# Optimization experiments

Hardware: AMD Instinct MI355X
Metric: run time of the kernel (lower is better)

The kernel has to match this reference:

```python
import jax, jax.numpy as jnp
import numpy as np

N_NODES = 10000   # chain length (supply-chain echelons)
BATCH   = 32      # graphs per batch
F_IN    = 5       # node features: inventory, replenishment, last_repl, units_sold, lost_sales
HID     = 128     # hidden_dim
LN_EPS  = 1e-5


def setup_inputs() -> dict:
    key = jax.random.key(0)
    ks = jax.random.split(key, 8)
    state  = jax.random.normal(ks[0], (BATCH, N_NODES * 4), dtype=jnp.float32)
    action = jax.random.normal(ks[1], (BATCH, N_NODES), dtype=jnp.float32)
    # GCNConv params (W: [F_IN, HID], bias added after aggregation, PyG convention)
    conv_w = jax.random.normal(ks[2], (F_IN, HID), dtype=jnp.float32) / np.sqrt(F_IN)
    conv_b = jax.random.normal(ks[3], (HID,), dtype=jnp.float32) * 0.01
    ln_g = jnp.ones((HID,), jnp.float32)
    ln_b = jnp.zeros((HID,), jnp.float32)
    w2 = jax.random.normal(ks[4], (HID, HID), dtype=jnp.float32) / np.sqrt(HID)
    b2 = jax.random.normal(ks[5], (HID,), dtype=jnp.float32) * 0.01
    w3 = jax.random.normal(ks[6], (HID, 1), dtype=jnp.float32) / np.sqrt(HID)
    b3 = jax.random.normal(ks[7], (1,), dtype=jnp.float32) * 0.01
    # bidirectional chain edges + self loops (GCNConv add_self_loops=True)
    i = np.arange(N_NODES)
    src = np.concatenate([i[:-1], i[1:], i]).astype(np.int32)
    dst = np.concatenate([i[1:], i[:-1], i]).astype(np.int32)
    return {
        "state": state, "action": action,
        "conv_w": conv_w, "conv_b": conv_b,
        "ln_g": ln_g, "ln_b": ln_b,
        "w2": w2, "b2": b2, "w3": w3, "b3": b3,
        "src": jnp.asarray(src), "dst": jnp.asarray(dst),
        "bs": BATCH,
    }


def reference(state, action, conv_w, conv_b, ln_g, ln_b, w2, b2, w3, b3, src, dst, bs):
    # sa = cat([state, action], -1), each batch row reshaped to [N_NODES, F_IN] node features
    sa = jnp.concatenate([state, action], axis=-1).reshape(bs, N_NODES, F_IN)

    # GCNConv: symmetric normalization with self-loops.
    deg = jnp.zeros((N_NODES,), sa.dtype).at[dst].add(1.0)      # in-degree incl. self-loop
    norm = jax.lax.rsqrt(deg[src] * deg[dst])                   # [E]

    h = jnp.einsum('bnf,fh->bnh', sa, conv_w)                   # transform first (F_IN small)
    msgs = h[:, src, :] * norm[None, :, None]                   # gather along edges [B,E,H]
    agg = jnp.zeros_like(h).at[:, dst, :].add(msgs)             # scatter-add aggregate [B,N,H]
    x = jax.nn.relu(agg + conv_b)

    # LayerNorm over feature dim
    mu = jnp.mean(x, axis=-1, keepdims=True)
    var = jnp.mean((x - mu) ** 2, axis=-1, keepdims=True)
    xn = (x - mu) * jax.lax.rsqrt(var + LN_EPS) * ln_g + ln_b

    # global_add_pool with batch vector of all zeros: sum over every node of the batched graph
    pooled = jnp.sum(xn, axis=(0, 1))[None, :]                  # [1, HID]

    y = jax.nn.relu(pooled @ w2 + b2)
    return y @ w3 + b3                                          # [1, 1]
```

## Files before the change

### kernel.cpp

```cpp
#include <hip/hip_runtime.h>
#include <math.h>

#define N_NODES 10000
#define BATCH   32
#define F_IN    5
#define HID     128
#define LN_EPS  1e-5f
#define CHUNK   500
#define NB_PER_BATCH 20
#define NBLK (BATCH * NB_PER_BATCH)
#define CONCAT_N (N_NODES * F_IN)
#define STATE_N  (N_NODES * 4)
#define STAGE_F4 635

__global__ __launch_bounds__(256) void gcn_ln_pool_kernel(
    const float* __restrict__ state, const float* __restrict__ action,
    const float* __restrict__ conv_w, const float* __restrict__ conv_b,
    float* __restrict__ partial)
{
    __shared__ float s_sa[2560];
    __shared__ float s_red[4][HID];

    const int b     = blockIdx.x / NB_PER_BATCH;
    const int chunk = blockIdx.x % NB_PER_BATCH;
    const int n0    = chunk * CHUNK;
    const int t     = threadIdx.x;

    const int e0 = (n0 - 4) * F_IN;
    const float4* stv = (const float4*)(state  + b * STATE_N);
    const float4* acv = (const float4*)(action + b * N_NODES);
    for (int i = t; i < STAGE_F4; i += 256) {
        const int e = e0 + i * 4;
        float4 v = make_float4(0.f, 0.f, 0.f, 0.f);
        if (e >= 0 && e < CONCAT_N)
            v = (e < STATE_N) ? stv[e >> 2] : acv[(e - STATE_N) >> 2];
        ((float4*)s_sa)[i] = v;
    }

    const int wave = t >> 6;
    const int lane = t & 63;
    const int s    = lane & 7;
    const int ng   = lane >> 3;

    float w[F_IN][16], cb[16];
#pragma unroll
    for (int j = 0; j < 16; ++j) {
        cb[j] = conv_b[s * 16 + j];
#pragma unroll
        for (int k = 0; k < F_IN; ++k) w[k][j] = conv_w[k * HID + s * 16 + j];
    }

    __syncthreads();

    float acc[16];
#pragma unroll
    for (int j = 0; j < 16; ++j) acc[j] = 0.f;
    float accS = 0.f;

    const float R33 = 1.f / 3.f;
    const float R23 = 0.40824829046386301637f;

    for (int sgi = wave; sgi < 8; sgi += 4) {
        const int loc1 = min(sgi * 64 + lane, CHUNK - 1);
        const int n    = n0 + loc1;
        const float wC = (n == 0 || n == N_NODES - 1) ? 0.5f : R33;
        const float wL = (n == 0) ? 0.f : ((n == 1 || n == N_NODES - 1) ? R23 : R33);
        const float wR = (n == N_NODES - 1) ? 0.f : ((n == N_NODES - 2 || n == 0) ? R23 : R33);
        const int li = (loc1 + 4) * F_IN;
        float sga[F_IN];
#pragma unroll
        for (int k = 0; k < F_IN; ++k)
            sga[k] = fmaf(s_sa[li - F_IN + k], wL,
                     fmaf(s_sa[li + k],        wC,
                          s_sa[li + F_IN + k] * wR));

        for (int sb = 0; sb < 8; ++sb) {
            const int src   = sb * 8 + ng;
            const int local = sgi * 64 + src;
            const bool valid = local < CHUNK;
            const float a0 = __shfl(sga[0], src);
            const float a1 = __shfl(sga[1], src);
            const float a2 = __shfl(sga[2], src);
            const float a3 = __shfl(sga[3], src);
            const float a4 = __shfl(sga[4], src);

            float v[16], sum = 0.f, sq = 0.f;
#pragma unroll
            for (int j = 0; j < 16; ++j) {
                float x = cb[j];
                x = fmaf(a0, w[0][j], x);
                x = fmaf(a1, w[1][j], x);
                x = fmaf(a2, w[2][j], x);
                x = fmaf(a3, w[3][j], x);
                x = fmaf(a4, w[4][j], x);
                x = fmaxf(x, 0.f);
                v[j] = x;
                sum += x;
                sq = fmaf(x, x, sq);
            }
#pragma unroll
            for (int m = 1; m < 8; m <<= 1) {
                sum += __shfl_xor(sum, m);
                sq  += __shfl_xor(sq, m);
            }
            const float mean = sum * (1.f / 128.f);
            const float var  = sq * (1.f / 128.f) - mean * mean;
            float r = rsqrtf(var + LN_EPS);
            r = valid ? r : 0.f;
#pragma unroll
            for (int j = 0; j < 16; ++j) acc[j] = fmaf(v[j], r, acc[j]);
            accS = fmaf(mean, r, accS);
        }
    }

#pragma unroll
    for (int m = 8; m < 64; m <<= 1) {
#pragma unroll
        for (int j = 0; j < 16; ++j) acc[j] += __shfl_xor(acc[j], m);
        accS += __shfl_xor(accS, m);
    }
    if (lane < 8) {
#pragma unroll
        for (int j = 0; j < 16; ++j) s_red[wave][lane * 16 + j] = acc[j] - accS;
    }
    __syncthreads();
    if (t < HID)
        partial[blockIdx.x * HID + t] =
            s_red[0][t] + s_red[1][t] + s_red[2][t] + s_red[3][t];
}

__global__ __launch_bounds__(1024) void reduce_mlp_kernel(
    const float* __restrict__ partial,
    const float* __restrict__ ln_g, const float* __restrict__ ln_b,
    const float* __restrict__ w2, const float* __restrict__ b2,
    const float* __restrict__ w3, const float* __restrict__ b3,
    float* __restrict__ out)
{
    __shared__ float s_red[8][HID];
    __shared__ float s_pool[HID];
    __shared__ float s_ws[2];
    const int t = threadIdx.x;
    const int f = t & 127, sl = t >> 7;

    float acc = 0.f;
#pragma unroll 8
    for (int r = sl; r < NBLK; r += 8) acc += partial[r * HID + f];
    s_red[sl][f] = acc;
    __syncthreads();

    if (t < HID) {
        float p = 0.f;
#pragma unroll
        for (int i = 0; i < 8; ++i) p += s_red[i][t];
        s_pool[t] = fmaf(ln_g[t], p, (float)(BATCH * N_NODES) * ln_b[t]);
    }
    __syncthreads();

    float yp = 0.f;
    const int k0 = sl * 16;
#pragma unroll
    for (int k = 0; k < 16; ++k) yp = fmaf(s_pool[k0 + k], w2[(k0 + k) * HID + f], yp);
    __syncthreads();
    s_red[sl][f] = yp;
    __syncthreads();

    if (t < HID) {
        float y = b2[t];
#pragma unroll
        for (int i = 0; i < 8; ++i) y += s_red[i][t];
        y = fmaxf(y, 0.f);
        float v = y * w3[t];
#pragma unroll
        for (int m = 1; m < 64; m <<= 1) v += __shfl_xor(v, m);
        if ((t & 63) == 0) s_ws[t >> 6] = v;
    }
    __syncthreads();
    if (t == 0) out[0] = s_ws[0] + s_ws[1] + b3[0];
}

extern "C" void kernel_launch(void* const* d_in, const int* in_sizes, int n_in,
                              void* d_out, int out_size, void* d_ws, size_t ws_size,
                              hipStream_t stream) {
    const float* state  = (const float*)d_in[0];
    const float* action = (const float*)d_in[1];
    const float* conv_w = (const float*)d_in[2];
    const float* conv_b = (const float*)d_in[3];
    const float* ln_g   = (const float*)d_in[4];
    const float* ln_b   = (const float*)d_in[5];
    const float* w2     = (const float*)d_in[6];
    const float* b2     = (const float*)d_in[7];
    const float* w3     = (const float*)d_in[8];
    const float* b3     = (const float*)d_in[9];
    float* partial = (float*)d_ws;

    gcn_ln_pool_kernel<<<NBLK, 256, 0, stream>>>(state, action, conv_w, conv_b, partial);
    reduce_mlp_kernel<<<1, 1024, 0, stream>>>(partial, ln_g, ln_b, w2, b2, w3, b3,
                                              (float*)d_out);
}
```

Baseline: 28.70 us.

## Fuse final reduction and MLP into main kernel via last-block atomic counter

Replaces the second single-block reduce/MLP kernel with a last-block-done pattern. Every block increments an atomic counter, and the block that finishes last sums the per-block partials and runs the MLP using its 256 threads. This removes one kernel launch and the gap between kernels, but adds a memset launch for the counter and runs the tail work on fewer threads.

```diff
diff --git a/kernel.cpp b/kernel.cpp
--- a/kernel.cpp
+++ b/kernel.cpp
@@ -12,14 +12,22 @@
 #define CONCAT_N (N_NODES * F_IN)
 #define STATE_N  (N_NODES * 4)
 #define STAGE_F4 635
-
-__global__ __launch_bounds__(256) void gcn_ln_pool_kernel(
+#define CTR_OFF  (512 * 1024)
+
+__global__ __launch_bounds__(256) void critic_fused_kernel(
     const float* __restrict__ state, const float* __restrict__ action,
     const float* __restrict__ conv_w, const float* __restrict__ conv_b,
-    float* __restrict__ partial)
+    const float* __restrict__ ln_g, const float* __restrict__ ln_b,
+    const float* __restrict__ w2, const float* __restrict__ b2,
+    const float* __restrict__ w3, const float* __restrict__ b3,
+    float* __restrict__ partial, unsigned int* __restrict__ counter,
+    float* __restrict__ out)
 {
     __shared__ float s_sa[2560];
-    __shared__ float s_red[4][HID];
+    __shared__ float s_red[8][HID];
+    __shared__ float s_pool[HID];
+    __shared__ float s_ws[2];
+    __shared__ bool  s_last;
 
     const int b     = blockIdx.x / NB_PER_BATCH;
     const int chunk = blockIdx.x % NB_PER_BATCH;
@@ -127,25 +135,28 @@
     if (t < HID)
         partial[blockIdx.x * HID + t] =
             s_red[0][t] + s_red[1][t] + s_red[2][t] + s_red[3][t];
-}
-
-__global__ __launch_bounds__(1024) void reduce_mlp_kernel(
-    const float* __restrict__ partial,
-    const float* __restrict__ ln_g, const float* __restrict__ ln_b,
-    const float* __restrict__ w2, const float* __restrict__ b2,
-    const float* __restrict__ w3, const float* __restrict__ b3,
-    float* __restrict__ out)
-{
-    __shared__ float s_red[8][HID];
-    __shared__ float s_pool[HID];
-    __shared__ float s_ws[2];
-    const int t = threadIdx.x;
-    const int f = t & 127, sl = t >> 7;
-
-    float acc = 0.f;
+
+    __threadfence();
+    __syncthreads();
+    if (t == 0)
+        s_last = (atomicAdd(counter, 1u) == NBLK - 1);
+    __syncthreads();
+    if (!s_last) return;
+    __threadfence();
+
+    const float4* p4 = (const float4*)partial;
+    const int c4  = t & 31;
+    const int sl8 = t >> 5;
+    float4 a = make_float4(0.f, 0.f, 0.f, 0.f);
 #pragma unroll 8
-    for (int r = sl; r < NBLK; r += 8) acc += partial[r * HID + f];
-    s_red[sl][f] = acc;
+    for (int r = sl8; r < NBLK; r += 8) {
+        const float4 v = p4[r * 32 + c4];
+        a.x += v.x; a.y += v.y; a.z += v.z; a.w += v.w;
+    }
+    s_red[sl8][c4 * 4 + 0] = a.x;
+    s_red[sl8][c4 * 4 + 1] = a.y;
+    s_red[sl8][c4 * 4 + 2] = a.z;
+    s_red[sl8][c4 * 4 + 3] = a.w;
     __syncthreads();
 
     if (t < HID) {
@@ -156,18 +167,18 @@
     }
     __syncthreads();
 
+    const int f  = t & 127;
+    const int k0 = (t >> 7) * 64;
     float yp = 0.f;
-    const int k0 = sl * 16;
-#pragma unroll
-    for (int k = 0; k < 16; ++k) yp = fmaf(s_pool[k0 + k], w2[(k0 + k) * HID + f], yp);
-    __syncthreads();
-    s_red[sl][f] = yp;
+#pragma unroll 8
+    for (int k = 0; k < 64; ++k)
+        yp = fmaf(s_pool[k0 + k], w2[(k0 + k) * HID + f], yp);
+    __syncthreads();
+    s_red[t >> 7][f] = yp;
     __syncthreads();
 
     if (t < HID) {
-        float y = b2[t];
-#pragma unroll
-        for (int i = 0; i < 8; ++i) y += s_red[i][t];
+        float y = b2[t] + s_red[0][t] + s_red[1][t];
         y = fmaxf(y, 0.f);
         float v = y * w3[t];
 #pragma unroll
@@ -192,8 +203,11 @@
     const float* w3     = (const float*)d_in[8];
     const float* b3     = (const float*)d_in[9];
     float* partial = (float*)d_ws;
-
-    gcn_ln_pool_kernel<<<NBLK, 256, 0, stream>>>(state, action, conv_w, conv_b, partial);
-    reduce_mlp_kernel<<<1, 1024, 0, stream>>>(partial, ln_g, ln_b, w2, b2, w3, b3,
-                                              (float*)d_out);
+    unsigned int* counter = (unsigned int*)((char*)d_ws + CTR_OFF);
+
+    hipMemsetAsync(counter, 0, sizeof(unsigned int), stream);
+
+    critic_fused_kernel<<<NBLK, 256, 0, stream>>>(state, action, conv_w, conv_b,
+                                                  ln_g, ln_b, w2, b2, w3, b3,
+                                                  partial, counter, (float*)d_out);
 }
```

After: 69.32 us. 142% more time.
